# Kernel tuning notes

Measured on AMD Instinct MI355X. Metric: run time of the kernel, lower is better.

## Reference

```python
import jax, jax.numpy as jnp
import numpy as np

N, E, D_IN, D, L = 50000, 800000, 128, 256, 3
BN_EPS = 1e-5


def _bn(x, gamma, beta):
    # torch BatchNorm1d training-mode forward: biased batch statistics over node dim
    m = x.mean(axis=0)
    v = x.var(axis=0)  # ddof=0, matches torch normalization
    return gamma * (x - m) * jax.lax.rsqrt(v + BN_EPS) + beta


def setup_inputs() -> dict:
    key = jax.random.key(0)
    ks = jax.random.split(key, 12)
    s_in = 1.0 / np.sqrt(D_IN)
    s_d = 1.0 / np.sqrt(D)
    s_2d = 1.0 / np.sqrt(2 * D)
    return {
        "pre_node_emb": jax.random.normal(ks[0], (1, N, D_IN), jnp.float32),
        "edge_index": jax.random.randint(ks[1], (1, E, 2), 0, N, jnp.int64),
        "W0": jax.random.uniform(ks[2], (D_IN, D), jnp.float32, -s_in, s_in),
        "b0": jax.random.uniform(ks[3], (D,), jnp.float32, -s_in, s_in),
        "W1": jax.random.uniform(ks[4], (L, D, 2 * D), jnp.float32, -s_d, s_d),
        "b1": jax.random.uniform(ks[5], (L, 2 * D), jnp.float32, -s_d, s_d),
        "g1": jnp.ones((L, 2 * D), jnp.float32),
        "beta1": jnp.zeros((L, 2 * D), jnp.float32),
        "W2": jax.random.uniform(ks[6], (L, 2 * D, D), jnp.float32, -s_2d, s_2d),
        "b2": jax.random.uniform(ks[7], (L, D), jnp.float32, -s_2d, s_2d),
        "gf": jnp.ones((L, D), jnp.float32),
        "betaf": jnp.zeros((L, D), jnp.float32),
    }


def reference(pre_node_emb, edge_index, W0, b0, W1, b1, g1, beta1, W2, b2, gf, betaf):
    x = pre_node_emb[0]            # [N, D_IN]
    ei = edge_index[0]             # [E, 2] -> transposed in torch; rows are (src, dst)
    src, dst = ei[:, 0], ei[:, 1]
    x = x @ W0 + b0                # node embedder -> [N, D]
    for l in range(L):
        # GINConv (eps=0): sum-aggregate neighbor messages, then MLP
        agg = jax.ops.segment_sum(x[src], dst, num_segments=N)   # scatter-add
        h = x + agg
        h = h @ W1[l] + b1[l]
        h = _bn(h, g1[l], beta1[l])
        h = jax.nn.relu(h)
        h = h @ W2[l] + b2[l]
        x = _bn(h + x, gf[l], betaf[l])  # residual + outer BatchNorm
    return x
```

## Files before the change

### kernel.cpp

```cpp
#include <hip/hip_runtime.h>

#define MNODES 50000
#define M_PAD  50048
#define NEDGES 800000
#define DIN    128
#define DD     256
#define D2     512
#define NLAYERS 3
#define BN_EPS 1e-5f

typedef unsigned short ushort_t;
typedef __bf16 v8bf __attribute__((ext_vector_type(8)));
typedef float  v4f  __attribute__((ext_vector_type(4)));

#define GLOBAL_AS __attribute__((address_space(1)))
#define LDS_AS    __attribute__((address_space(3)))

__device__ __forceinline__ float bf2f(ushort_t u) {
    unsigned x = ((unsigned)u) << 16;
    return __uint_as_float(x);
}
__device__ __forceinline__ ushort_t f2bf(float f) {
    unsigned u = __float_as_uint(f);
    u += 0x7FFF + ((u >> 16) & 1);
    return (ushort_t)(u >> 16);
}
__device__ __forceinline__ void async16(const ushort_t* g, ushort_t* l) {
    __builtin_amdgcn_global_load_lds((const GLOBAL_AS unsigned int*)g,
                                     (LDS_AS unsigned int*)l, 16, 0, 0);
}

#define R0 (M_PAD * DIN)
#define RW (DIN * DD + 2 * NLAYERS * DD * D2)
__global__ void k_prep_all(const float* __restrict__ pre, ushort_t* __restrict__ preb,
                           const float* __restrict__ W0, const float* __restrict__ W1,
                           const float* __restrict__ W2,
                           ushort_t* __restrict__ W0T, ushort_t* __restrict__ W1T,
                           ushort_t* __restrict__ W2T,
                           float* __restrict__ caf, float* __restrict__ ccf,
                           float* __restrict__ sums1, float* __restrict__ sumsF,
                           int* __restrict__ deg) {
    int i = blockIdx.x * blockDim.x + threadIdx.x;
    if (i < R0) {
        int row = i >> 7;
        preb[i] = f2bf(row < MNODES ? pre[i] : 0.f);
        return;
    }
    int j = i - R0;
    if (j < RW) {
        if (j < DIN * DD) {
            int n = j >> 7, k = j & 127;
            W0T[j] = f2bf(W0[k * DD + n]);
        } else if (j < DIN * DD + NLAYERS * DD * D2) {
            int j2 = j - DIN * DD;
            int l = j2 >> 17, off = j2 & 131071;
            int n = off >> 8, k = off & 255;
            W1T[(size_t)l * 131072 + off] = f2bf(W1[(size_t)l * 131072 + k * D2 + n]);
        } else {
            int j2 = j - DIN * DD - NLAYERS * DD * D2;
            int l = j2 >> 17, off = j2 & 131071;
            int n = off >> 9, k = off & 511;
            W2T[(size_t)l * 131072 + off] = f2bf(W2[(size_t)l * 131072 + k * DD + n]);
        }
        return;
    }
    j -= RW;
    if (j < 256) { caf[j] = 1.f; ccf[j] = 0.f; return; }
    j -= 256;
    if (j < 1024) { sums1[j] = 0.f; return; }
    j -= 1024;
    if (j < 512) { sumsF[j] = 0.f; return; }
    j -= 512;
    if (j < MNODES) deg[j] = 0;
}

__global__ void k_hist(const int* __restrict__ ei, int* __restrict__ deg) {
    int e = blockIdx.x * blockDim.x + threadIdx.x;
    if (e < NEDGES) atomicAdd(&deg[ei[e * 2 + 1]], 1);
}
__global__ void k_scan1(const int* __restrict__ deg, int* __restrict__ rowptr,
                        int* __restrict__ bsum, int n) {
    __shared__ int tmp[256];
    int tid = threadIdx.x;
    int i = blockIdx.x * 256 + tid;
    int v = (i < n) ? deg[i] : 0;
    tmp[tid] = v;
    __syncthreads();
    #pragma unroll
    for (int off = 1; off < 256; off <<= 1) {
        int t = (tid >= off) ? tmp[tid - off] : 0;
        __syncthreads();
        tmp[tid] += t;
        __syncthreads();
    }
    if (i < n) rowptr[i + 1] = tmp[tid];
    if (tid == 255) bsum[blockIdx.x] = tmp[255];
}
__global__ __launch_bounds__(256)
void k_scan2(int* __restrict__ bsum, int nb) {
    __shared__ int tmp[256];
    int tid = threadIdx.x;
    int v = (tid < nb) ? bsum[tid] : 0;
    tmp[tid] = v;
    __syncthreads();
    #pragma unroll
    for (int off = 1; off < 256; off <<= 1) {
        int t = (tid >= off) ? tmp[tid - off] : 0;
        __syncthreads();
        tmp[tid] += t;
        __syncthreads();
    }
    if (tid < nb) bsum[tid] = tmp[tid] - v;
}
__global__ void k_scan3(const int* __restrict__ deg, const int* __restrict__ bsum,
                        int* __restrict__ rowptr, int* __restrict__ cursor, int n) {
    int i = blockIdx.x * 256 + threadIdx.x;
    if (i == 0) rowptr[0] = 0;
    if (i < n) {
        int incl = rowptr[i + 1] + bsum[i >> 8];
        rowptr[i + 1] = incl;
        cursor[i] = incl - deg[i];
    }
}
__global__ void k_fill(const int* __restrict__ ei, int* __restrict__ cursor,
                       int* __restrict__ col) {
    int e = blockIdx.x * blockDim.x + threadIdx.x;
    if (e < NEDGES) {
        int pos = atomicAdd(&cursor[ei[e * 2 + 1]], 1);
        col[pos] = ei[e * 2];
    }
}

__global__ void k_gather(const int* __restrict__ rowptr, const int* __restrict__ col,
                         const ushort_t* __restrict__ x, const float* __restrict__ ca,
                         const float* __restrict__ cc, ushort_t* __restrict__ out) {
    int node = blockIdx.x * 4 + (threadIdx.x >> 6);
    int lane = threadIdx.x & 63;
    if (node >= MNODES) return;
    const ushort4* xp = (const ushort4*)x;
    ushort4 v = xp[(size_t)node * 64 + lane];
    float a0 = bf2f(v.x), a1 = bf2f(v.y), a2 = bf2f(v.z), a3 = bf2f(v.w);
    int s = rowptr[node], e = rowptr[node + 1];
    int i = s;
    for (; i + 3 < e; i += 4) {
        ushort4 u0 = xp[(size_t)col[i]     * 64 + lane];
        ushort4 u1 = xp[(size_t)col[i + 1] * 64 + lane];
        ushort4 u2 = xp[(size_t)col[i + 2] * 64 + lane];
        ushort4 u3 = xp[(size_t)col[i + 3] * 64 + lane];
        a0 += bf2f(u0.x) + bf2f(u1.x) + bf2f(u2.x) + bf2f(u3.x);
        a1 += bf2f(u0.y) + bf2f(u1.y) + bf2f(u2.y) + bf2f(u3.y);
        a2 += bf2f(u0.z) + bf2f(u1.z) + bf2f(u2.z) + bf2f(u3.z);
        a3 += bf2f(u0.w) + bf2f(u1.w) + bf2f(u2.w) + bf2f(u3.w);
    }
    for (; i < e; i++) {
        ushort4 u = xp[(size_t)col[i] * 64 + lane];
        a0 += bf2f(u.x); a1 += bf2f(u.y); a2 += bf2f(u.z); a3 += bf2f(u.w);
    }
    int c = lane * 4;
    float dn = (float)(e - s) + 1.0f;
    ushort4 o;
    o.x = f2bf(ca[c + 0] * a0 + dn * cc[c + 0]);
    o.y = f2bf(ca[c + 1] * a1 + dn * cc[c + 1]);
    o.z = f2bf(ca[c + 2] * a2 + dn * cc[c + 2]);
    o.w = f2bf(ca[c + 3] * a3 + dn * cc[c + 3]);
    ((ushort4*)out)[(size_t)node * 64 + lane] = o;
}

__global__ void k_coeffs(float* __restrict__ sums, float* __restrict__ sumsq,
                         const float* __restrict__ g, const float* __restrict__ beta,
                         float* __restrict__ ca, float* __restrict__ cc, int n) {
    int c = blockIdx.x * blockDim.x + threadIdx.x;
    if (c >= n) return;
    float mean = sums[c] * (1.0f / MNODES);
    float var  = sumsq[c] * (1.0f / MNODES) - mean * mean;
    float a    = g[c] * rsqrtf(var + BN_EPS);
    ca[c] = a;
    cc[c] = beta[c] - a * mean;
    sums[c] = 0.f;
    sumsq[c] = 0.f;
}

__global__ void k_prerelu(ushort_t* __restrict__ h, const float* __restrict__ ca,
                          const float* __restrict__ cc) {
    int i = blockIdx.x * blockDim.x + threadIdx.x;
    if (i >= MNODES * (D2 / 4)) return;
    int c = (i * 4) & (D2 - 1);
    ushort4 v = ((const ushort4*)h)[i];
    ushort4 o;
    o.x = f2bf(fmaxf(ca[c + 0] * bf2f(v.x) + cc[c + 0], 0.f));
    o.y = f2bf(fmaxf(ca[c + 1] * bf2f(v.y) + cc[c + 1], 0.f));
    o.z = f2bf(fmaxf(ca[c + 2] * bf2f(v.z) + cc[c + 2], 0.f));
    o.w = f2bf(fmaxf(ca[c + 3] * bf2f(v.w) + cc[c + 3], 0.f));
    ((ushort4*)h)[i] = o;
}

__global__ void k_apply_out(const ushort_t* __restrict__ h, const float* __restrict__ ca,
                            const float* __restrict__ cc, float* __restrict__ out) {
    int i = blockIdx.x * blockDim.x + threadIdx.x;
    if (i >= MNODES * 64) return;
    int c = (i & 63) * 4;
    ushort4 v = ((const ushort4*)h)[i];
    float4 o;
    o.x = ca[c + 0] * bf2f(v.x) + cc[c + 0];
    o.y = ca[c + 1] * bf2f(v.y) + cc[c + 1];
    o.z = ca[c + 2] * bf2f(v.z) + cc[c + 2];
    o.w = ca[c + 3] * bf2f(v.w) + cc[c + 3];
    ((float4*)out)[i] = o;
}

template<int DO_STATS, int RES>
__global__ __launch_bounds__(256)
void k_gemm_bf(const ushort_t* __restrict__ A, const ushort_t* __restrict__ WT,
               const float* __restrict__ bias,
               const ushort_t* resid, const float* __restrict__ r_ca,
               const float* __restrict__ r_cc,
               ushort_t* out, float* __restrict__ sums, float* __restrict__ sumsq,
               int M, int K, int N) {
    __shared__ ushort_t As[128 * 64];
    __shared__ ushort_t Bs[128 * 64];
    const int tid = threadIdx.x;
    const int w = tid >> 6, lane = tid & 63;
    const int wm = w >> 1, wn = w & 1;
    const int quad = lane >> 4, l15 = lane & 15;
    const int m0 = blockIdx.y * 128, n0 = blockIdx.x * 128;

    v4f acc[4][4];
    #pragma unroll
    for (int i = 0; i < 4; i++)
        #pragma unroll
        for (int j = 0; j < 4; j++)
            acc[i][j] = (v4f){0.f, 0.f, 0.f, 0.f};

    for (int kt = 0; kt < K; kt += 64) {
        #pragma unroll
        for (int i = 0; i < 4; i++) {
            int rblk = i * 4 + w;
            int r = rblk * 8 + (lane >> 3);
            int cg = (lane & 7) ^ (r & 7);
            async16(A + (size_t)(m0 + r) * K + kt + cg * 8, &As[rblk * 512]);
        }
        #pragma unroll
        for (int i = 0; i < 4; i++) {
            int rblk = i * 4 + w;
            int r = rblk * 8 + (lane >> 3);
            int cg = (lane & 7) ^ (r & 7);
            async16(WT + (size_t)(n0 + r) * K + kt + cg * 8, &Bs[rblk * 512]);
        }
        __syncthreads();
        #pragma unroll
        for (int ks = 0; ks < 2; ks++) {
            v8bf af[4], bfr[4];
            int cl = (ks * 4 + quad) ^ (l15 & 7);
            #pragma unroll
            for (int t = 0; t < 4; t++) {
                int m_l = wm * 64 + t * 16 + l15;
                af[t] = *(const v8bf*)&As[m_l * 64 + cl * 8];
                int n_l = wn * 64 + t * 16 + l15;
                bfr[t] = *(const v8bf*)&Bs[n_l * 64 + cl * 8];
            }
            #pragma unroll
            for (int mt = 0; mt < 4; mt++)
                #pragma unroll
                for (int nt = 0; nt < 4; nt++)
                    acc[mt][nt] = __builtin_amdgcn_mfma_f32_16x16x32_bf16(
                        af[mt], bfr[nt], acc[mt][nt], 0, 0, 0);
        }
        __syncthreads();
    }

    const int mlim = M - m0;
    float s_sum[4] = {0.f, 0.f, 0.f, 0.f}, s_sq[4] = {0.f, 0.f, 0.f, 0.f};
    #pragma unroll
    for (int nt = 0; nt < 4; nt++) {
        int colg = n0 + wn * 64 + nt * 16 + l15;
        float bia = bias[colg];
        float rca = 0.f, rcc = 0.f;
        if (RES) { rca = r_ca[colg]; rcc = r_cc[colg]; }
        #pragma unroll
        for (int mt = 0; mt < 4; mt++) {
            int rbase = wm * 64 + mt * 16 + quad * 4;
            #pragma unroll
            for (int r = 0; r < 4; r++) {
                int rl = rbase + r;
                if (rl < mlim) {
                    size_t idx = (size_t)(m0 + rl) * N + colg;
                    float v = acc[mt][nt][r] + bia;
                    if (RES) v += rca * bf2f(resid[idx]) + rcc;
                    out[idx] = f2bf(v);
                    if (DO_STATS) { s_sum[nt] += v; s_sq[nt] += v * v; }
                }
            }
        }
    }
    if (DO_STATS) {
        #pragma unroll
        for (int nt = 0; nt < 4; nt++) {
            float s = s_sum[nt], q = s_sq[nt];
            s += __shfl_xor(s, 16); q += __shfl_xor(q, 16);
            s += __shfl_xor(s, 32); q += __shfl_xor(q, 32);
            if (quad == 0) {
                int colg = n0 + wn * 64 + nt * 16 + l15;
                atomicAdd(&sums[colg], s);
                atomicAdd(&sumsq[colg], q);
            }
        }
    }
}

extern "C" void kernel_launch(void* const* d_in, const int* in_sizes, int n_in,
                              void* d_out, int out_size, void* d_ws, size_t ws_size,
                              hipStream_t stream) {
    const float* pre   = (const float*)d_in[0];
    const int*   ei    = (const int*)d_in[1];
    const float* W0    = (const float*)d_in[2];
    const float* b0    = (const float*)d_in[3];
    const float* W1    = (const float*)d_in[4];
    const float* b1    = (const float*)d_in[5];
    const float* g1    = (const float*)d_in[6];
    const float* beta1 = (const float*)d_in[7];
    const float* W2    = (const float*)d_in[8];
    const float* b2    = (const float*)d_in[9];
    const float* gf    = (const float*)d_in[10];
    const float* betaf = (const float*)d_in[11];

    char* p = (char*)d_ws;
    ushort_t* preb = (ushort_t*)p; p += (size_t)M_PAD * DIN * 2;
    ushort_t* ACT1 = (ushort_t*)p; p += (size_t)M_PAD * DD * 2;
    ushort_t* ACT2 = (ushort_t*)p; p += (size_t)M_PAD * DD * 2;
    ushort_t* H1   = (ushort_t*)p; p += (size_t)M_PAD * D2 * 2;
    ushort_t* W0T  = (ushort_t*)p; p += (size_t)DIN * DD * 2;
    ushort_t* W1T  = (ushort_t*)p; p += (size_t)NLAYERS * DD * D2 * 2;
    ushort_t* W2T  = (ushort_t*)p; p += (size_t)NLAYERS * D2 * DD * 2;
    float* sums1  = (float*)p; p += D2 * 4;
    float* sumsq1 = (float*)p; p += D2 * 4;
    float* ca1    = (float*)p; p += D2 * 4;
    float* cc1    = (float*)p; p += D2 * 4;
    float* sumsF  = (float*)p; p += DD * 4;
    float* sumsqF = (float*)p; p += DD * 4;
    float* caf    = (float*)p; p += DD * 4;
    float* ccf    = (float*)p; p += DD * 4;
    int* deg    = (int*)p; p += (size_t)MNODES * 4;
    int* rowptr = (int*)p; p += (size_t)(MNODES + 1) * 4;
    int* cursor = (int*)p; p += (size_t)MNODES * 4;
    int* colx   = (int*)p; p += (size_t)NEDGES * 4;
    int* bsum   = (int*)p; p += 256 * 4;

    dim3 blk(256);
    const int mb = (MNODES + 127) / 128;
    const int nsb = (MNODES + 255) / 256;

    const int prep_total = R0 + RW + 256 + 1024 + 512 + MNODES;
    k_prep_all<<<(prep_total + 255) / 256, blk, 0, stream>>>(
        pre, preb, W0, W1, W2, W0T, W1T, W2T, caf, ccf, sums1, sumsF, deg);

    k_hist<<<(NEDGES + 255) / 256, blk, 0, stream>>>(ei, deg);
    k_scan1<<<nsb, blk, 0, stream>>>(deg, rowptr, bsum, MNODES);
    k_scan2<<<1, blk, 0, stream>>>(bsum, nsb);
    k_scan3<<<nsb, blk, 0, stream>>>(deg, bsum, rowptr, cursor, MNODES);
    k_fill<<<(NEDGES + 255) / 256, blk, 0, stream>>>(ei, cursor, colx);

    k_gemm_bf<0, 0><<<dim3(DD / 128, mb), blk, 0, stream>>>(
        preb, W0T, b0, nullptr, nullptr, nullptr, ACT2, nullptr, nullptr,
        MNODES, DIN, DD);

    for (int l = 0; l < NLAYERS; l++) {
        k_gather<<<(MNODES + 3) / 4, blk, 0, stream>>>(rowptr, colx, ACT2, caf, ccf, ACT1);

        k_gemm_bf<1, 0><<<dim3(D2 / 128, mb), blk, 0, stream>>>(
            ACT1, W1T + (size_t)l * DD * D2, b1 + (size_t)l * D2,
            nullptr, nullptr, nullptr, H1, sums1, sumsq1, MNODES, DD, D2);
        k_coeffs<<<2, blk, 0, stream>>>(sums1, sumsq1, g1 + (size_t)l * D2,
                                        beta1 + (size_t)l * D2, ca1, cc1, D2);

        k_prerelu<<<(MNODES * (D2 / 4) + 255) / 256, blk, 0, stream>>>(H1, ca1, cc1);

        k_gemm_bf<1, 1><<<dim3(DD / 128, mb), blk, 0, stream>>>(
            H1, W2T + (size_t)l * D2 * DD, b2 + (size_t)l * DD,
            ACT2, caf, ccf, ACT2, sumsF, sumsqF, MNODES, D2, DD);
        k_coeffs<<<1, blk, 0, stream>>>(sumsF, sumsqF, gf + (size_t)l * DD,
                                        betaf + (size_t)l * DD, caf, ccf, DD);
    }

    k_apply_out<<<(MNODES * 64 + 255) / 256, blk, 0, stream>>>(ACT2, caf, ccf, (float*)d_out);
}
```

Measured before the change: 861.8 us.

## Fuse BN+ReLU into second GEMM A-load and software-pipeline GEMM with register prefetch

Result: slower. 963.5 us (+11.8%).

```diff
diff --git a/kernel.cpp b/kernel.cpp
--- a/kernel.cpp
+++ b/kernel.cpp
@@ -13,9 +13,6 @@
 typedef __bf16 v8bf __attribute__((ext_vector_type(8)));
 typedef float  v4f  __attribute__((ext_vector_type(4)));
 
-#define GLOBAL_AS __attribute__((address_space(1)))
-#define LDS_AS    __attribute__((address_space(3)))
-
 __device__ __forceinline__ float bf2f(ushort_t u) {
     unsigned x = ((unsigned)u) << 16;
     return __uint_as_float(x);
@@ -25,9 +22,8 @@
     u += 0x7FFF + ((u >> 16) & 1);
     return (ushort_t)(u >> 16);
 }
-__device__ __forceinline__ void async16(const ushort_t* g, ushort_t* l) {
-    __builtin_amdgcn_global_load_lds((const GLOBAL_AS unsigned int*)g,
-                                     (LDS_AS unsigned int*)l, 16, 0, 0);
+__device__ __forceinline__ void softbarrier() {
+    asm volatile("s_waitcnt lgkmcnt(0)\n\ts_barrier" ::: "memory");
 }
 
 #define R0 (M_PAD * DIN)
@@ -180,20 +176,6 @@
     sumsq[c] = 0.f;
 }
 
-__global__ void k_prerelu(ushort_t* __restrict__ h, const float* __restrict__ ca,
-                          const float* __restrict__ cc) {
-    int i = blockIdx.x * blockDim.x + threadIdx.x;
-    if (i >= MNODES * (D2 / 4)) return;
-    int c = (i * 4) & (D2 - 1);
-    ushort4 v = ((const ushort4*)h)[i];
-    ushort4 o;
-    o.x = f2bf(fmaxf(ca[c + 0] * bf2f(v.x) + cc[c + 0], 0.f));
-    o.y = f2bf(fmaxf(ca[c + 1] * bf2f(v.y) + cc[c + 1], 0.f));
-    o.z = f2bf(fmaxf(ca[c + 2] * bf2f(v.z) + cc[c + 2], 0.f));
-    o.w = f2bf(fmaxf(ca[c + 3] * bf2f(v.w) + cc[c + 3], 0.f));
-    ((ushort4*)h)[i] = o;
-}
-
 __global__ void k_apply_out(const ushort_t* __restrict__ h, const float* __restrict__ ca,
                             const float* __restrict__ cc, float* __restrict__ out) {
     int i = blockIdx.x * blockDim.x + threadIdx.x;
@@ -208,22 +190,56 @@
     ((float4*)out)[i] = o;
 }
 
-template<int DO_STATS, int RES>
+__device__ __forceinline__ uint4 bn_relu_pack(uint4 v, const float* pca,
+                                              const float* pcc, int kb) {
+    uint4 o;
+    #pragma unroll
+    for (int d = 0; d < 4; d++) {
+        unsigned x = ((const unsigned*)&v)[d];
+        float lo = bf2f((ushort_t)(x & 0xFFFF));
+        float hi = bf2f((ushort_t)(x >> 16));
+        lo = fmaxf(pca[kb + 2 * d] * lo + pcc[kb + 2 * d], 0.f);
+        hi = fmaxf(pca[kb + 2 * d + 1] * hi + pcc[kb + 2 * d + 1], 0.f);
+        ((unsigned*)&o)[d] = (unsigned)f2bf(lo) | ((unsigned)f2bf(hi) << 16);
+    }
+    return o;
+}
+
+template<int DO_STATS, int RES, int PRE>
 __global__ __launch_bounds__(256)
 void k_gemm_bf(const ushort_t* __restrict__ A, const ushort_t* __restrict__ WT,
                const float* __restrict__ bias,
                const ushort_t* resid, const float* __restrict__ r_ca,
                const float* __restrict__ r_cc,
+               const float* __restrict__ p_ca, const float* __restrict__ p_cc,
                ushort_t* out, float* __restrict__ sums, float* __restrict__ sumsq,
                int M, int K, int N) {
-    __shared__ ushort_t As[128 * 64];
-    __shared__ ushort_t Bs[128 * 64];
+    __shared__ ushort_t As[2][128 * 64];
+    __shared__ ushort_t Bs[2][128 * 64];
+    __shared__ float spca[PRE ? 512 : 1];
+    __shared__ float spcc[PRE ? 512 : 1];
+
     const int tid = threadIdx.x;
     const int w = tid >> 6, lane = tid & 63;
     const int wm = w >> 1, wn = w & 1;
     const int quad = lane >> 4, l15 = lane & 15;
     const int m0 = blockIdx.y * 128, n0 = blockIdx.x * 128;
 
+    const int r_in = lane >> 3;
+    const int s_slot = lane & 7;
+    const int cg = s_slot ^ r_in;
+    const ushort_t* aA[4];
+    const ushort_t* aB[4];
+    int ldsoff[4];
+    #pragma unroll
+    for (int i = 0; i < 4; i++) {
+        int rblk = i * 4 + w;
+        int r = rblk * 8 + r_in;
+        aA[i] = A  + (size_t)(m0 + r) * K + cg * 8;
+        aB[i] = WT + (size_t)(n0 + r) * K + cg * 8;
+        ldsoff[i] = rblk * 512 + r_in * 64 + s_slot * 8;
+    }
+
     v4f acc[4][4];
     #pragma unroll
     for (int i = 0; i < 4; i++)
@@ -231,32 +247,61 @@
         for (int j = 0; j < 4; j++)
             acc[i][j] = (v4f){0.f, 0.f, 0.f, 0.f};
 
-    for (int kt = 0; kt < K; kt += 64) {
+    const int nk = K >> 6;
+    uint4 ar[4], br[4];
+
+    if (PRE) {
+        for (int i = tid; i < K; i += 256) { spca[i] = p_ca[i]; spcc[i] = p_cc[i]; }
+    }
+    #pragma unroll
+    for (int i = 0; i < 4; i++) { ar[i] = *(const uint4*)aA[i]; br[i] = *(const uint4*)aB[i]; }
+    if (PRE) __syncthreads();
+    #pragma unroll
+    for (int i = 0; i < 4; i++) {
+        uint4 va = PRE ? bn_relu_pack(ar[i], spca, spcc, cg * 8) : ar[i];
+        *(uint4*)&As[0][ldsoff[i]] = va;
+        *(uint4*)&Bs[0][ldsoff[i]] = br[i];
+    }
+    if (nk > 1) {
         #pragma unroll
         for (int i = 0; i < 4; i++) {
-            int rblk = i * 4 + w;
-            int r = rblk * 8 + (lane >> 3);
-            int cg = (lane & 7) ^ (r & 7);
-            async16(A + (size_t)(m0 + r) * K + kt + cg * 8, &As[rblk * 512]);
-        }
-        #pragma unroll
-        for (int i = 0; i < 4; i++) {
-            int rblk = i * 4 + w;
-            int r = rblk * 8 + (lane >> 3);
-            int cg = (lane & 7) ^ (r & 7);
-            async16(WT + (size_t)(n0 + r) * K + kt + cg * 8, &Bs[rblk * 512]);
-        }
-        __syncthreads();
+            ar[i] = *(const uint4*)(aA[i] + 64);
+            br[i] = *(const uint4*)(aB[i] + 64);
+        }
+    }
+    softbarrier();
+
+    for (int t = 0; t < nk; t++) {
+        if (t + 1 < nk) {
+            int buf = (t + 1) & 1;
+            int kw = (t + 1) * 64;
+            #pragma unroll
+            for (int i = 0; i < 4; i++) {
+                uint4 va = PRE ? bn_relu_pack(ar[i], spca, spcc, kw + cg * 8) : ar[i];
+                *(uint4*)&As[buf][ldsoff[i]] = va;
+                *(uint4*)&Bs[buf][ldsoff[i]] = br[i];
+            }
+            if (t + 2 < nk) {
+                int kl = (t + 2) * 64;
+                #pragma unroll
+                for (int i = 0; i < 4; i++) {
+                    ar[i] = *(const uint4*)(aA[i] + kl);
+                    br[i] = *(const uint4*)(aB[i] + kl);
+                }
+            }
+        }
+        const ushort_t* Ab = As[t & 1];
+        const ushort_t* Bb = Bs[t & 1];
         #pragma unroll
         for (int ks = 0; ks < 2; ks++) {
             v8bf af[4], bfr[4];
             int cl = (ks * 4 + quad) ^ (l15 & 7);
             #pragma unroll
-            for (int t = 0; t < 4; t++) {
-                int m_l = wm * 64 + t * 16 + l15;
-                af[t] = *(const v8bf*)&As[m_l * 64 + cl * 8];
-                int n_l = wn * 64 + t * 16 + l15;
-                bfr[t] = *(const v8bf*)&Bs[n_l * 64 + cl * 8];
+            for (int tt = 0; tt < 4; tt++) {
+                int m_l = wm * 64 + tt * 16 + l15;
+                af[tt] = *(const v8bf*)&Ab[m_l * 64 + cl * 8];
+                int n_l = wn * 64 + tt * 16 + l15;
+                bfr[tt] = *(const v8bf*)&Bb[n_l * 64 + cl * 8];
             }
             #pragma unroll
             for (int mt = 0; mt < 4; mt++)
@@ -265,7 +310,7 @@
                     acc[mt][nt] = __builtin_amdgcn_mfma_f32_16x16x32_bf16(
                         af[mt], bfr[nt], acc[mt][nt], 0, 0, 0);
         }
-        __syncthreads();
+        softbarrier();
     }
 
     const int mlim = M - m0;
@@ -359,24 +404,24 @@
     k_scan3<<<nsb, blk, 0, stream>>>(deg, bsum, rowptr, cursor, MNODES);
     k_fill<<<(NEDGES + 255) / 256, blk, 0, stream>>>(ei, cursor, colx);
 
-    k_gemm_bf<0, 0><<<dim3(DD / 128, mb), blk, 0, stream>>>(
-        preb, W0T, b0, nullptr, nullptr, nullptr, ACT2, nullptr, nullptr,
-        MNODES, DIN, DD);
+    k_gemm_bf<0, 0, 0><<<dim3(DD / 128, mb), blk, 0, stream>>>(
+        preb, W0T, b0, nullptr, nullptr, nullptr, nullptr, nullptr,
+        ACT2, nullptr, nullptr, MNODES, DIN, DD);
 
     for (int l = 0; l < NLAYERS; l++) {
         k_gather<<<(MNODES + 3) / 4, blk, 0, stream>>>(rowptr, colx, ACT2, caf, ccf, ACT1);
 
-        k_gemm_bf<1, 0><<<dim3(D2 / 128, mb), blk, 0, stream>>>(
+        k_gemm_bf<1, 0, 0><<<dim3(D2 / 128, mb), blk, 0, stream>>>(
             ACT1, W1T + (size_t)l * DD * D2, b1 + (size_t)l * D2,
-            nullptr, nullptr, nullptr, H1, sums1, sumsq1, MNODES, DD, D2);
+            nullptr, nullptr, nullptr, nullptr, nullptr,
+            H1, sums1, sumsq1, MNODES, DD, D2);
         k_coeffs<<<2, blk, 0, stream>>>(sums1, sumsq1, g1 + (size_t)l * D2,
                                         beta1 + (size_t)l * D2, ca1, cc1, D2);
 
-        k_prerelu<<<(MNODES * (D2 / 4) + 255) / 256, blk, 0, stream>>>(H1, ca1, cc1);
-
-        k_gemm_bf<1, 1><<<dim3(DD / 128, mb), blk, 0, stream>>>(
+        k_gemm_bf<1, 1, 1><<<dim3(DD / 128, mb), blk, 0, stream>>>(
             H1, W2T + (size_t)l * D2 * DD, b2 + (size_t)l * DD,
-            ACT2, caf, ccf, ACT2, sumsF, sumsqF, MNODES, D2, DD);
+            ACT2, caf, ccf, ca1, cc1,
+            ACT2, sumsF, sumsqF, MNODES, D2, DD);
         k_coeffs<<<1, blk, 0, stream>>>(sumsF, sumsqF, gf + (size_t)l * DD,
                                         betaf + (size_t)l * DD, caf, ccf, DD);
     }
```

## Double-buffer GEMM LDS tiles with async prefetch and unroll gather by eight

Applied to the files above, without the earlier changes.

After: 807.3 us. 1.07x faster.

```diff
diff --git a/kernel.cpp b/kernel.cpp
--- a/kernel.cpp
+++ b/kernel.cpp
@@ -29,6 +29,9 @@
     __builtin_amdgcn_global_load_lds((const GLOBAL_AS unsigned int*)g,
                                      (LDS_AS unsigned int*)l, 16, 0, 0);
 }
+#define BARRIER() asm volatile("s_barrier" ::: "memory")
+#define VMWAIT4() asm volatile("s_waitcnt vmcnt(4)" ::: "memory")
+#define VMWAIT0() asm volatile("s_waitcnt vmcnt(0)" ::: "memory")
 
 #define R0 (M_PAD * DIN)
 #define RW (DIN * DD + 2 * NLAYERS * DD * D2)
@@ -142,15 +145,15 @@
     float a0 = bf2f(v.x), a1 = bf2f(v.y), a2 = bf2f(v.z), a3 = bf2f(v.w);
     int s = rowptr[node], e = rowptr[node + 1];
     int i = s;
-    for (; i + 3 < e; i += 4) {
-        ushort4 u0 = xp[(size_t)col[i]     * 64 + lane];
-        ushort4 u1 = xp[(size_t)col[i + 1] * 64 + lane];
-        ushort4 u2 = xp[(size_t)col[i + 2] * 64 + lane];
-        ushort4 u3 = xp[(size_t)col[i + 3] * 64 + lane];
-        a0 += bf2f(u0.x) + bf2f(u1.x) + bf2f(u2.x) + bf2f(u3.x);
-        a1 += bf2f(u0.y) + bf2f(u1.y) + bf2f(u2.y) + bf2f(u3.y);
-        a2 += bf2f(u0.z) + bf2f(u1.z) + bf2f(u2.z) + bf2f(u3.z);
-        a3 += bf2f(u0.w) + bf2f(u1.w) + bf2f(u2.w) + bf2f(u3.w);
+    for (; i + 7 < e; i += 8) {
+        ushort4 u[8];
+        #pragma unroll
+        for (int j = 0; j < 8; j++) u[j] = xp[(size_t)col[i + j] * 64 + lane];
+        #pragma unroll
+        for (int j = 0; j < 8; j++) {
+            a0 += bf2f(u[j].x); a1 += bf2f(u[j].y);
+            a2 += bf2f(u[j].z); a3 += bf2f(u[j].w);
+        }
     }
     for (; i < e; i++) {
         ushort4 u = xp[(size_t)col[i] * 64 + lane];
@@ -209,21 +212,34 @@
 }
 
 template<int DO_STATS, int RES>
-__global__ __launch_bounds__(256)
+__global__ __launch_bounds__(256, 4)
 void k_gemm_bf(const ushort_t* __restrict__ A, const ushort_t* __restrict__ WT,
                const float* __restrict__ bias,
                const ushort_t* resid, const float* __restrict__ r_ca,
                const float* __restrict__ r_cc,
                ushort_t* out, float* __restrict__ sums, float* __restrict__ sumsq,
                int M, int K, int N) {
-    __shared__ ushort_t As[128 * 64];
-    __shared__ ushort_t Bs[128 * 64];
+    __shared__ __align__(16) ushort_t As[2][128 * 32];
+    __shared__ __align__(16) ushort_t Bs[2][128 * 32];
     const int tid = threadIdx.x;
     const int w = tid >> 6, lane = tid & 63;
     const int wm = w >> 1, wn = w & 1;
     const int quad = lane >> 4, l15 = lane & 15;
     const int m0 = blockIdx.y * 128, n0 = blockIdx.x * 128;
 
+    const ushort_t* aA[2];
+    const ushort_t* aB[2];
+    int aoff[2];
+    #pragma unroll
+    for (int j = 0; j < 2; j++) {
+        int ii = j * 4 + w;
+        int r = ii * 16 + (lane >> 2);
+        int cg = (lane & 3) ^ ((r >> 2) & 3);
+        aA[j] = A  + (size_t)(m0 + r) * K + cg * 8;
+        aB[j] = WT + (size_t)(n0 + r) * K + cg * 8;
+        aoff[j] = ii * 512;
+    }
+
     v4f acc[4][4];
     #pragma unroll
     for (int i = 0; i < 4; i++)
@@ -231,41 +247,53 @@
         for (int j = 0; j < 4; j++)
             acc[i][j] = (v4f){0.f, 0.f, 0.f, 0.f};
 
-    for (int kt = 0; kt < K; kt += 64) {
-        #pragma unroll
-        for (int i = 0; i < 4; i++) {
-            int rblk = i * 4 + w;
-            int r = rblk * 8 + (lane >> 3);
-            int cg = (lane & 7) ^ (r & 7);
-            async16(A + (size_t)(m0 + r) * K + kt + cg * 8, &As[rblk * 512]);
-        }
-        #pragma unroll
-        for (int i = 0; i < 4; i++) {
-            int rblk = i * 4 + w;
-            int r = rblk * 8 + (lane >> 3);
-            int cg = (lane & 7) ^ (r & 7);
-            async16(WT + (size_t)(n0 + r) * K + kt + cg * 8, &Bs[rblk * 512]);
-        }
-        __syncthreads();
-        #pragma unroll
-        for (int ks = 0; ks < 2; ks++) {
-            v8bf af[4], bfr[4];
-            int cl = (ks * 4 + quad) ^ (l15 & 7);
+    const int nk = K >> 5;
+
+    #pragma unroll
+    for (int j = 0; j < 2; j++) {
+        async16(aA[j], &As[0][aoff[j]]);
+        async16(aB[j], &Bs[0][aoff[j]]);
+    }
+    #pragma unroll
+    for (int j = 0; j < 2; j++) {
+        async16(aA[j] + 32, &As[1][aoff[j]]);
+        async16(aB[j] + 32, &Bs[1][aoff[j]]);
+    }
+    VMWAIT4();
+    BARRIER();
+
+    const int sl = quad ^ ((l15 >> 2) & 3);
+    for (int t = 0; t < nk; t++) {
+        const ushort_t* Ab = As[t & 1];
+        const ushort_t* Bb = Bs[t & 1];
+        v8bf af[4], bfr[4];
+        #pragma unroll
+        for (int tt = 0; tt < 4; tt++) {
+            int m_l = wm * 64 + tt * 16 + l15;
+            af[tt]  = *(const v8bf*)&Ab[m_l * 32 + sl * 8];
+            int n_l = wn * 64 + tt * 16 + l15;
+            bfr[tt] = *(const v8bf*)&Bb[n_l * 32 + sl * 8];
+        }
+        #pragma unroll
+        for (int mt = 0; mt < 4; mt++)
             #pragma unroll
-            for (int t = 0; t < 4; t++) {
-                int m_l = wm * 64 + t * 16 + l15;
-                af[t] = *(const v8bf*)&As[m_l * 64 + cl * 8];
-                int n_l = wn * 64 + t * 16 + l15;
-                bfr[t] = *(const v8bf*)&Bs[n_l * 64 + cl * 8];
+            for (int nt = 0; nt < 4; nt++)
+                acc[mt][nt] = __builtin_amdgcn_mfma_f32_16x16x32_bf16(
+                    af[mt], bfr[nt], acc[mt][nt], 0, 0, 0);
+        if (t == nk - 1) break;
+        BARRIER();
+        if (t + 2 < nk) {
+            int kl = (t + 2) * 32;
+            #pragma unroll
+            for (int j = 0; j < 2; j++) {
+                async16(aA[j] + kl, &As[t & 1][aoff[j]]);
+                async16(aB[j] + kl, &Bs[t & 1][aoff[j]]);
             }
-            #pragma unroll
-            for (int mt = 0; mt < 4; mt++)
-                #pragma unroll
-                for (int nt = 0; nt < 4; nt++)
-                    acc[mt][nt] = __builtin_amdgcn_mfma_f32_16x16x32_bf16(
-                        af[mt], bfr[nt], acc[mt][nt], 0, 0, 0);
-        }
-        __syncthreads();
+            VMWAIT4();
+        } else {
+            VMWAIT0();
+        }
+        BARRIER();
     }
 
     const int mlim = M - m0;
@@ -360,15 +388,16 @@
     k_fill<<<(NEDGES + 255) / 256, blk, 0, stream>>>(ei, cursor, colx);
 
     k_gemm_bf<0, 0><<<dim3(DD / 128, mb), blk, 0, stream>>>(
-        preb, W0T, b0, nullptr, nullptr, nullptr, ACT2, nullptr, nullptr,
-        MNODES, DIN, DD);
+        preb, W0T, b0, nullptr, nullptr, nullptr,
+        ACT2, nullptr, nullptr, MNODES, DIN, DD);
 
     for (int l = 0; l < NLAYERS; l++) {
         k_gather<<<(MNODES + 3) / 4, blk, 0, stream>>>(rowptr, colx, ACT2, caf, ccf, ACT1);
 
         k_gemm_bf<1, 0><<<dim3(D2 / 128, mb), blk, 0, stream>>>(
             ACT1, W1T + (size_t)l * DD * D2, b1 + (size_t)l * D2,
-            nullptr, nullptr, nullptr, H1, sums1, sumsq1, MNODES, DD, D2);
+            nullptr, nullptr, nullptr,
+            H1, sums1, sumsq1, MNODES, DD, D2);
         k_coeffs<<<2, blk, 0, stream>>>(sums1, sumsq1, g1 + (size_t)l * D2,
                                         beta1 + (size_t)l * D2, ca1, cc1, D2);
 
@@ -376,7 +405,8 @@
 
         k_gemm_bf<1, 1><<<dim3(DD / 128, mb), blk, 0, stream>>>(
             H1, W2T + (size_t)l * D2 * DD, b2 + (size_t)l * DD,
-            ACT2, caf, ccf, ACT2, sumsF, sumsqF, MNODES, D2, DD);
+            ACT2, caf, ccf,
+            ACT2, sumsF, sumsqF, MNODES, D2, DD);
         k_coeffs<<<1, blk, 0, stream>>>(sumsF, sumsqF, gf + (size_t)l * DD,
                                         betaf + (size_t)l * DD, caf, ccf, DD);
     }
```
